# Performance work log

Hardware: AMD Instinct MI355X
Metric: run time of the kernel (lower is better)

## Reference

```python
import jax, jax.numpy as jnp
import numpy as np

CHUNK = 32
H = 4

def silu(x):
    return x * jax.nn.sigmoid(x)

def l2norm(x):
    return x * jax.lax.rsqrt(jnp.sum(x * x, -1, keepdims=True) + 1e-6)

def dwconv_causal(x_cl, w):
    # x_cl: (b, C, L), w: (C, k) depthwise causal conv (cross-correlation, left pad k-1)
    k = w.shape[1]
    xp = jnp.pad(x_cl, ((0, 0), (0, 0), (k - 1, 0)))
    return jax.lax.conv_general_dilated(xp, w[:, None, :], (1,), 'VALID',
        dimension_numbers=('NCH', 'OIH', 'NCH'), feature_group_count=x_cl.shape[1])

def short_conv_silu(x_bld, w):
    y = dwconv_causal(jnp.swapaxes(x_bld, 1, 2), w)
    return silu(jnp.swapaxes(y, 1, 2))

def delta_rule_chunkwise(q, k, v, beta, chunk=CHUNK):
    # q,k: (b,h,L,dk)  v: (b,h,L,dv)  beta: (b,h,L)
    b, h, L, dk = q.shape
    dv = v.shape[-1]
    pad = (-L) % chunk
    if pad:
        q, k, v = (jnp.pad(t, ((0, 0), (0, 0), (0, pad), (0, 0))) for t in (q, k, v))
        beta = jnp.pad(beta, ((0, 0), (0, 0), (0, pad)))
    n = (L + pad) // chunk
    q = l2norm(q)
    k = l2norm(k)
    v = v * beta[..., None]
    kb = k * beta[..., None]
    ch = lambda x: x.reshape(b, h, n, chunk, x.shape[-1])
    qc, kc, vc, kbc = map(ch, (q, k, v, kb))
    idx = jnp.arange(chunk)
    strict_lower = (idx[:, None] > idx[None, :]).astype(q.dtype)
    incl_lower = (idx[:, None] >= idx[None, :]).astype(q.dtype)
    # forward substitution to invert (I - tril(beta K K^T, -1)) per chunk
    attn = -jnp.einsum('bhncd,bhned->bhnce', kbc, kc) * strict_lower
    for i in range(1, chunk):
        upd = jnp.einsum('...j,...ji->...i', attn[..., i, :], attn[..., :, :i])
        attn = attn.at[..., i, :i].add(upd)
    attn = attn + jnp.eye(chunk, dtype=q.dtype)
    u = attn @ vc          # (b,h,n,c,dv)
    w = attn @ kbc         # (b,h,n,c,dk)
    xs = tuple(jnp.moveaxis(t, 2, 0) for t in (qc, kc, u, w))
    S0 = jnp.zeros((b, h, dk, dv), q.dtype)
    def step(S, x):
        qi, ki, ui, wi = x
        a_loc = jnp.einsum('bhcd,bhed->bhce', qi, ki) * incl_lower
        ui = ui - wi @ S
        oi = qi @ S + a_loc @ ui
        S = S + jnp.einsum('bhcd,bhcv->bhdv', ki, ui)
        return S, oi
    S, o = jax.lax.scan(step, S0, xs)
    o = jnp.moveaxis(o, 0, 2).reshape(b, h, n * chunk, dv)[:, :, :L]
    return o, S

def multiscale_conv(v, ms_w3, ms_w15, ms_w31, kernel_mix_w, channel_mixer_w):
    # v: (b,l,h,d)
    b, l, h, d = v.shape
    x = jnp.swapaxes(v.reshape(b, l, h * d), 1, 2)  # (b, h*d, l)
    outs = [dwconv_causal(x, w) for w in (ms_w3, ms_w15, ms_w31)]
    y = jnp.concatenate(outs, axis=1)               # (b, 3*h*d, l)
    # faithful to torch rearrange 'b (h kd) l -> b l h kd' on the concat layout
    y = y.reshape(b, h, 3 * d, l).transpose(0, 3, 1, 2)  # (b,l,h,3d)
    y = y @ kernel_mix_w                            # (b,l,h,d)
    y = (y.reshape(b, l, h * d) @ channel_mixer_w).reshape(b, l, h, d)
    return y

def _forward(hidden_states, Wq, Wk, Wv, Wb, conv_q_w, conv_k_w, conv_v_w,
             ms_w3, ms_w15, ms_w31, kernel_mix_w, channel_mixer_w,
             fusion_w1, fusion_b1, fusion_w2, fusion_b2, o_norm_w, Wo):
    b, L, D = hidden_states.shape
    h = H
    dk = Wq.shape[1] // h
    dv = Wv.shape[1] // h
    q = short_conv_silu(hidden_states @ Wq, conv_q_w).reshape(b, L, h, dk)
    k = short_conv_silu(hidden_states @ Wk, conv_k_w).reshape(b, L, h, dk)
    v = short_conv_silu(hidden_states @ Wv, conv_v_w).reshape(b, L, h, dv)
    v_direct = v
    beta = jax.nn.sigmoid(hidden_states @ Wb)  # (b,L,h)
    tr = lambda x: jnp.swapaxes(x, 1, 2)
    delta_out, _S = delta_rule_chunkwise(tr(q), tr(k), tr(v), tr(beta))
    delta_out = jnp.swapaxes(delta_out, 1, 2)  # (b,L,h,dv)
    ms_out = multiscale_conv(v_direct, ms_w3, ms_w15, ms_w31, kernel_mix_w, channel_mixer_w)
    bn = lambda x: jnp.mean(jnp.abs(x), -1)    # (b,L,h)
    gate_features = jnp.concatenate([hidden_states, bn(ms_out), bn(delta_out), bn(v_direct)], -1)
    hdn = jax.nn.gelu(gate_features @ fusion_w1 + fusion_b1, approximate=False)
    logits = (hdn @ fusion_w2 + fusion_b2).reshape(b, L, h, 3)
    wts = jax.nn.softmax(logits, -1)
    o = wts[..., 0:1] * ms_out + wts[..., 1:2] * delta_out + wts[..., 2:3] * v_direct
    o = o * jax.lax.rsqrt(jnp.mean(o * o, -1, keepdims=True) + 1e-5) * o_norm_w  # RMSNorm
    return o.reshape(b, L, h * dv) @ Wo

def setup_inputs() -> dict:
    B, L, D = 4, 2048, 1024
    h, d = H, D // H
    key = jax.random.key(0)
    ks = jax.random.split(key, 20)
    nrm = lambda k, shp, s: (jax.random.normal(k, shp, dtype=jnp.float32) * s)
    inp = {
        'hidden_states': nrm(ks[0], (B, L, D), 1.0),
        'Wq': nrm(ks[1], (D, D), D ** -0.5),
        'Wk': nrm(ks[2], (D, D), D ** -0.5),
        'Wv': nrm(ks[3], (D, D), D ** -0.5),
        'Wb': nrm(ks[4], (D, h), D ** -0.5),
        'conv_q_w': nrm(ks[5], (D, 4), 0.3),
        'conv_k_w': nrm(ks[6], (D, 4), 0.3),
        'conv_v_w': nrm(ks[7], (D, 4), 0.3),
        'ms_w3': nrm(ks[8], (D, 3), 0.02),
        'ms_w15': nrm(ks[9], (D, 15), 0.02),
        'ms_w31': nrm(ks[10], (D, 31), 0.02),
        'kernel_mix_w': nrm(ks[11], (3 * d, d), (3 * d) ** -0.5),
        'channel_mixer_w': nrm(ks[12], (D, D), D ** -0.5),
        'fusion_w1': nrm(ks[13], (D + 3 * h, 2 * D), (D + 3 * h) ** -0.5),
        'fusion_b1': jnp.zeros((2 * D,), jnp.float32),
        'fusion_w2': nrm(ks[14], (2 * D, 3 * h), (2 * D) ** -0.5),
        'fusion_b2': jnp.concatenate([jnp.zeros((2 * h,), jnp.float32), jnp.ones((h,), jnp.float32)]),
        'o_norm_w': jnp.ones((d,), jnp.float32),
        'Wo': nrm(ks[15], (D, D), D ** -0.5),
    }
    return inp

def reference(hidden_states, Wq, Wk, Wv, Wb, conv_q_w, conv_k_w, conv_v_w,
              ms_w3, ms_w15, ms_w31, kernel_mix_w, channel_mixer_w,
              fusion_w1, fusion_b1, fusion_w2, fusion_b2, o_norm_w, Wo):
    return _forward(hidden_states, Wq, Wk, Wv, Wb, conv_q_w, conv_k_w, conv_v_w,
                    ms_w3, ms_w15, ms_w31, kernel_mix_w, channel_mixer_w,
                    fusion_w1, fusion_b1, fusion_w2, fusion_b2, o_norm_w, Wo)
```

## Files before the change

kernel.cpp:

```cpp
#include <hip/hip_runtime.h>
#include <math.h>


typedef __attribute__((ext_vector_type(8))) __bf16 bf16x8;
typedef __attribute__((ext_vector_type(4))) float f32x4;

__device__ inline ushort f2bf(float f) {
    union { float f; unsigned u; } x; x.f = f;
    unsigned u = x.u;
    u += 0x7fffu + ((u >> 16) & 1u);
    return (ushort)(u >> 16);
}
__device__ inline float bf2f(ushort h) {
    union { unsigned u; float f; } x; x.u = ((unsigned)h) << 16;
    return x.f;
}
__device__ inline float ldf(float v) { return v; }
__device__ inline float ldf(ushort v) { return bf2f(v); }

template<int EPI>
__global__ __launch_bounds__(256) void gemm_mfma(
    const ushort* __restrict__ A, const ushort* __restrict__ BT,
    const float* __restrict__ bias, const float* __restrict__ extA,
    const float* __restrict__ extB, void* __restrict__ Cout,
    int M, int N, int K)
{
    __shared__ ushort As[2][128 * 32];
    __shared__ ushort Bs[2][128 * 32];
    __shared__ float bns[(EPI >= 2) ? 128 * 13 : 1];
    __shared__ float exb[(EPI >= 2) ? 12 * 128 : 1];
    const int tid = threadIdx.x;
    const int row0 = blockIdx.y * 128, col0 = blockIdx.x * 128;
    const int lane = tid & 63, wave = tid >> 6;
    const int wr = (wave >> 1) * 64, wc = (wave & 1) * 64;

    if (EPI >= 2) {
        for (int e = tid; e < 128 * 12; e += 256)
            bns[(e / 12) * 13 + (e % 12)] = extA[(long)(row0 + e / 12) * 12 + e % 12];
        for (int e = tid; e < 12 * 128; e += 256)
            exb[e] = extB[(long)(e >> 7) * N + col0 + (e & 127)];
    }

    f32x4 acc[4][4];
    #pragma unroll
    for (int m = 0; m < 4; ++m)
        #pragma unroll
        for (int n = 0; n < 4; ++n) {
            acc[m][n][0] = 0.f; acc[m][n][1] = 0.f;
            acc[m][n][2] = 0.f; acc[m][n][3] = 0.f;
        }

    const int rA = lane & 15;
    const int ko = (lane >> 4) * 8;
    const int srow = tid >> 2;
    const int skk = (tid & 3) * 8;

    for (int k0 = 0; k0 < K; k0 += 64) {
        #pragma unroll
        for (int hf = 0; hf < 2; ++hf) {
            #pragma unroll
            for (int i = 0; i < 2; ++i) {
                const long ga = (long)(row0 + i * 64 + srow) * K + k0 + hf * 32 + skk;
                __builtin_amdgcn_global_load_lds(
                    (const __attribute__((address_space(1))) void*)(A + ga),
                    (__attribute__((address_space(3))) void*)(&As[hf][0] + i * 2048 + wave * 512),
                    16, 0, 0);
                const long gb = (long)(col0 + i * 64 + srow) * K + k0 + hf * 32 + skk;
                __builtin_amdgcn_global_load_lds(
                    (const __attribute__((address_space(1))) void*)(BT + gb),
                    (__attribute__((address_space(3))) void*)(&Bs[hf][0] + i * 2048 + wave * 512),
                    16, 0, 0);
            }
        }
        __syncthreads();
        #pragma unroll
        for (int hf = 0; hf < 2; ++hf) {
            bf16x8 af[4], bfr[4];
            #pragma unroll
            for (int m = 0; m < 4; ++m)
                af[m] = *(const bf16x8*)(&As[hf][0] + (wr + m * 16 + rA) * 32 + ko);
            #pragma unroll
            for (int n = 0; n < 4; ++n)
                bfr[n] = *(const bf16x8*)(&Bs[hf][0] + (wc + n * 16 + rA) * 32 + ko);
            #pragma unroll
            for (int m = 0; m < 4; ++m)
                #pragma unroll
                for (int n = 0; n < 4; ++n)
                    acc[m][n] = __builtin_amdgcn_mfma_f32_16x16x32_bf16(af[m], bfr[n], acc[m][n], 0, 0, 0);
        }
        __syncthreads();
    }

    const int crow = (lane >> 4) * 4;
    const int ccol = lane & 15;
    #pragma unroll
    for (int m = 0; m < 4; ++m) {
        #pragma unroll
        for (int n = 0; n < 4; ++n) {
            #pragma unroll
            for (int r = 0; r < 4; ++r) {
                const int rl = wr + m * 16 + crow + r;
                const int cl = wc + n * 16 + ccol;
                float vv = acc[m][n][r];
                if (EPI >= 2) {
                    vv += bias[col0 + cl];
                    #pragma unroll
                    for (int j = 0; j < 12; ++j) vv += bns[rl * 13 + j] * exb[j * 128 + cl];
                    vv = 0.5f * vv * (1.f + erff(vv * 0.70710678118654752f));
                }
                const long off = (long)(row0 + rl) * N + col0 + cl;
                if (EPI == 0) ((float*)Cout)[off] = vv;
                else ((ushort*)Cout)[off] = f2bf(vv);
            }
        }
    }
}

__global__ __launch_bounds__(256) void transpose_cast(const float* __restrict__ W,
    ushort* __restrict__ WT, int K, int N)
{
    __shared__ float t[32][33];
    const int k0 = blockIdx.y * 32, n0 = blockIdx.x * 32;
    const int c = threadIdx.x & 31, r8 = threadIdx.x >> 5;
    #pragma unroll
    for (int rr = 0; rr < 4; ++rr) {
        const int r = r8 + rr * 8;
        t[r][c] = W[(long)(k0 + r) * N + n0 + c];
    }
    __syncthreads();
    #pragma unroll
    for (int rr = 0; rr < 4; ++rr) {
        const int r = r8 + rr * 8;
        WT[(long)(n0 + r) * K + k0 + c] = f2bf(t[c][r]);
    }
}

__global__ __launch_bounds__(256) void cast_bf16(const float* __restrict__ x,
    ushort* __restrict__ y)
{
    const long i = ((long)blockIdx.x * 256 + threadIdx.x) * 4;
    const float4 v = *(const float4*)(x + i);
    ushort4 o;
    o.x = f2bf(v.x); o.y = f2bf(v.y); o.z = f2bf(v.z); o.w = f2bf(v.w);
    *(ushort4*)(y + i) = o;
}

template<int NOUT, int MODE, typename TA>
__global__ __launch_bounds__(256) void gemm_smallN(const TA* __restrict__ A,
    const float* __restrict__ Bm, const float* __restrict__ bias,
    float* __restrict__ Cm, int K)
{
    __shared__ float part[4][NOUT];
    __shared__ float sm[NOUT];
    const int m = blockIdx.x, tid = threadIdx.x;
    const TA* ar = A + (long)m * K;
    float acc[NOUT];
    #pragma unroll
    for (int j = 0; j < NOUT; ++j) acc[j] = 0.f;
    for (int k = tid; k < K; k += 256) {
        const float a = ldf(ar[k]);
        #pragma unroll
        for (int j = 0; j < NOUT; ++j) acc[j] += a * Bm[(long)k * NOUT + j];
    }
    #pragma unroll
    for (int j = 0; j < NOUT; ++j)
        for (int off = 32; off > 0; off >>= 1) acc[j] += __shfl_down(acc[j], off);
    const int wid = tid >> 6, lane = tid & 63;
    if (lane == 0) {
        #pragma unroll
        for (int j = 0; j < NOUT; ++j) part[wid][j] = acc[j];
    }
    __syncthreads();
    if (tid < NOUT) {
        float s = part[0][tid] + part[1][tid] + part[2][tid] + part[3][tid];
        if (MODE == 0) {
            Cm[(long)m * NOUT + tid] = 1.f / (1.f + expf(-s));
        } else {
            sm[tid] = s + bias[tid];
        }
    }
    if (MODE == 1) {
        __syncthreads();
        if (tid < NOUT) {
            const int hh = tid / 3, r = tid - hh * 3;
            const float a0 = sm[hh * 3], a1 = sm[hh * 3 + 1], a2 = sm[hh * 3 + 2];
            const float mx = fmaxf(a0, fmaxf(a1, a2));
            const float e0 = expf(a0 - mx), e1 = expf(a1 - mx), e2 = expf(a2 - mx);
            const float mine = (r == 0) ? e0 : ((r == 1) ? e1 : e2);
            Cm[(long)m * NOUT + tid] = mine / (e0 + e1 + e2);
        }
    }
}

__global__ __launch_bounds__(256) void conv4_silu(const float* __restrict__ x,
    const float* __restrict__ wc, float* __restrict__ y)
{
    const long idx = (long)blockIdx.x * 256 + threadIdx.x;
    const int c = (int)(idx & 1023);
    const long bl = idx >> 10;
    const int l = (int)(bl & 2047);
    const long b = bl >> 11;
    const float* xp = x + b * 2048 * 1024 + c;
    const float* wp = wc + c * 4;
    float s = 0.f;
    #pragma unroll
    for (int t = 0; t < 4; ++t) {
        const int ll = l - 3 + t;
        if (ll >= 0) s += xp[(long)ll * 1024] * wp[t];
    }
    y[idx] = s / (1.f + expf(-s));
}

__global__ __launch_bounds__(256) void l2norm_bf16(const float* __restrict__ x,
    ushort* __restrict__ y)
{
    const long wid = ((long)blockIdx.x * 256 + threadIdx.x) >> 6;
    const int lane = threadIdx.x & 63;
    const float4 xv = *(const float4*)(x + wid * 256 + lane * 4);
    float ss = xv.x * xv.x + xv.y * xv.y + xv.z * xv.z + xv.w * xv.w;
    for (int off = 32; off > 0; off >>= 1) ss += __shfl_down(ss, off);
    ss = __shfl(ss, 0);
    const float inv = rsqrtf(ss + 1e-6f);
    ushort4 o;
    o.x = f2bf(xv.x * inv); o.y = f2bf(xv.y * inv);
    o.z = f2bf(xv.z * inv); o.w = f2bf(xv.w * inv);
    *(ushort4*)(y + wid * 256 + lane * 4) = o;
}

__global__ __launch_bounds__(256) void chunk_prep(
    const ushort* __restrict__ qn, const ushort* __restrict__ kn,
    const float* __restrict__ v, const float* __restrict__ beta,
    float* __restrict__ u, ushort* __restrict__ w16,
    ushort* __restrict__ kT16, ushort* __restrict__ al16)
{
    __shared__ float kb_s[32 * 256];
    __shared__ float bufB[32 * 256];
    __shared__ float Ms[32 * 33];
    __shared__ float Rs[32 * 33];
    __shared__ float bet[32];
    const int blk = blockIdx.x;
    const int n = blk & 63;
    const int bh = blk >> 6;
    const int h = bh & 3;
    const int b = bh >> 2;
    const int tid = threadIdx.x;
    const long lbase = (long)b * 2048 + n * 32;

    if (tid < 32) bet[tid] = beta[(lbase + tid) * 4 + h];
    __syncthreads();
    for (int e = tid; e < 8192; e += 256) {
        const int c = e >> 8, dd = e & 255;
        const float kv = bf2f(kn[(lbase + c) * 1024 + h * 256 + dd]);
        bufB[dd * 32 + c] = kv;
        kb_s[c * 256 + dd] = kv * bet[c];
    }
    __syncthreads();
    for (int e = tid; e < 8192; e += 256)
        kT16[(long)blk * 8192 + e] = f2bf(bufB[e]);

    const int j = tid & 31, i0 = tid >> 5;
    {
        float m4[4] = {0.f, 0.f, 0.f, 0.f};
        for (int dd = 0; dd < 256; ++dd) {
            const float kt = bufB[dd * 32 + j];
            #pragma unroll
            for (int ii = 0; ii < 4; ++ii) m4[ii] += kb_s[(i0 + 8 * ii) * 256 + dd] * kt;
        }
        #pragma unroll
        for (int ii = 0; ii < 4; ++ii) {
            const int i = i0 + 8 * ii;
            const float mv = (i > j) ? -m4[ii] : 0.f;
            Ms[i * 33 + j] = mv;
            Rs[i * 33 + j] = mv + ((i == j) ? 1.f : 0.f);
        }
    }
    {
        float a4[4] = {0.f, 0.f, 0.f, 0.f};
        for (int dd = 0; dd < 256; ++dd) {
            const float kt = bufB[dd * 32 + j];
            #pragma unroll
            for (int ii = 0; ii < 4; ++ii)
                a4[ii] += bf2f(qn[(lbase + (i0 + 8 * ii)) * 1024 + h * 256 + dd]) * kt;
        }
        #pragma unroll
        for (int ii = 0; ii < 4; ++ii) {
            const int i = i0 + 8 * ii;
            al16[(long)blk * 1024 + i * 32 + j] = f2bf((i >= j) ? a4[ii] : 0.f);
        }
    }
    __syncthreads();
    for (int it = 0; it < 4; ++it) {
        float p4[4] = {0.f, 0.f, 0.f, 0.f};
        for (int kk = 0; kk < 32; ++kk) {
            const float pb = Ms[kk * 33 + j];
            #pragma unroll
            for (int ii = 0; ii < 4; ++ii) p4[ii] += Ms[(i0 + 8 * ii) * 33 + kk] * pb;
        }
        __syncthreads();
        #pragma unroll
        for (int ii = 0; ii < 4; ++ii) Ms[(i0 + 8 * ii) * 33 + j] = p4[ii];
        __syncthreads();
        float r4[4] = {0.f, 0.f, 0.f, 0.f};
        for (int kk = 0; kk < 32; ++kk) {
            const float pb = Ms[kk * 33 + j];
            #pragma unroll
            for (int ii = 0; ii < 4; ++ii) r4[ii] += Rs[(i0 + 8 * ii) * 33 + kk] * pb;
        }
        __syncthreads();
        #pragma unroll
        for (int ii = 0; ii < 4; ++ii) Rs[(i0 + 8 * ii) * 33 + j] += r4[ii];
        __syncthreads();
    }
    for (int e = tid; e < 8192; e += 256) {
        const int c = e >> 8, dd = e & 255;
        bufB[c * 256 + dd] = v[(lbase + c) * 1024 + h * 256 + dd] * bet[c];
    }
    __syncthreads();
    {
        const int dd = tid;
        float accU[32], accW[32];
        #pragma unroll
        for (int r = 0; r < 32; ++r) { accU[r] = 0.f; accW[r] = 0.f; }
        for (int kk = 0; kk < 32; ++kk) {
            const float vv = bufB[kk * 256 + dd];
            const float bb = kb_s[kk * 256 + dd];
            #pragma unroll
            for (int r = 0; r < 32; ++r) {
                const float rr = Rs[r * 33 + kk];
                accU[r] += rr * vv;
                accW[r] += rr * bb;
            }
        }
        const long base = (long)blk * 32;
        #pragma unroll
        for (int r = 0; r < 32; ++r) {
            u  [(base + r) * 256 + dd] = accU[r];
            w16[(base + r) * 256 + dd] = f2bf(accW[r]);
        }
    }
}

__global__ __launch_bounds__(64, 1) void delta_scan_mfma(
    const ushort* __restrict__ q16, const ushort* __restrict__ kT16,
    const ushort* __restrict__ w16, const float* __restrict__ u,
    const ushort* __restrict__ al16, float* __restrict__ dt)
{
    __shared__ __align__(16) ushort Sb[16 * 264];
    __shared__ __align__(16) ushort Ub[16 * 40];
    const int blk = blockIdx.x;
    const int bh = blk & 15;
    const int sl = blk >> 4;
    const int h = bh & 3;
    const int b = bh >> 2;
    const int v0 = sl * 16;
    const int lane = threadIdx.x;
    const int col = lane & 15;
    const int grp = lane >> 4;

    const ushort* wp  = w16  + ((long)bh * 64 * 32 + col) * 256 + grp * 8;
    const ushort* qp  = q16  + ((long)b * 2048 + col) * 1024 + h * 256 + grp * 8;
    const ushort* kp  = kT16 + ((long)bh * 64 * 256 + col) * 32 + grp * 8;
    const ushort* ap  = al16 + ((long)bh * 64 * 32 + col) * 32 + grp * 8;
    const float*  Ug  = u    + ((long)bh * 64 * 32 + grp * 4) * 256 + v0 + col;
    float*        dp  = dt   + ((long)b * 2048 + grp * 4) * 1024 + h * 256 + v0 + col;

    f32x4 S[16];
    #pragma unroll
    for (int t = 0; t < 16; ++t) { S[t][0] = 0.f; S[t][1] = 0.f; S[t][2] = 0.f; S[t][3] = 0.f; }

    bf16x8 wf[2][8], qf[2][8], kf[16], alf[2], sf[8];
    float upre[8];

    #pragma unroll
    for (int kb = 0; kb < 8; ++kb)
        #pragma unroll
        for (int e = 0; e < 8; ++e) sf[kb][e] = (__bf16)0.f;

    #pragma unroll
    for (int rt = 0; rt < 2; ++rt)
        #pragma unroll
        for (int kb = 0; kb < 8; ++kb) {
            wf[rt][kb] = *(const bf16x8*)(wp + rt * 4096 + kb * 32);
            qf[rt][kb] = *(const bf16x8*)(qp + (long)rt * 16384 + kb * 32);
        }
    #pragma unroll
    for (int t = 0; t < 16; ++t) kf[t] = *(const bf16x8*)(kp + t * 512);
    alf[0] = *(const bf16x8*)(ap);
    alf[1] = *(const bf16x8*)(ap + 512);
    #pragma unroll
    for (int rt = 0; rt < 2; ++rt)
        #pragma unroll
        for (int r = 0; r < 4; ++r)
            upre[rt * 4 + r] = Ug[rt * 4096 + r * 256];

    for (int n = 0; n < 64; ++n) {
        f32x4 up[2];
        #pragma unroll
        for (int rt = 0; rt < 2; ++rt) {
            f32x4 a; a[0] = 0.f; a[1] = 0.f; a[2] = 0.f; a[3] = 0.f;
            #pragma unroll
            for (int kb = 0; kb < 8; ++kb)
                a = __builtin_amdgcn_mfma_f32_16x16x32_bf16(wf[rt][kb], sf[kb], a, 0, 0, 0);
            #pragma unroll
            for (int r = 0; r < 4; ++r)
                up[rt][r] = upre[rt * 4 + r] - a[r];
        }
        if (n < 63) {
            #pragma unroll
            for (int rt = 0; rt < 2; ++rt)
                #pragma unroll
                for (int kb = 0; kb < 8; ++kb)
                    wf[rt][kb] = *(const bf16x8*)(wp + (long)(n + 1) * 8192 + rt * 4096 + kb * 32);
        }

        #pragma unroll
        for (int rt = 0; rt < 2; ++rt) {
            ushort4 p;
            p.x = f2bf(up[rt][0]); p.y = f2bf(up[rt][1]);
            p.z = f2bf(up[rt][2]); p.w = f2bf(up[rt][3]);
            *(ushort4*)&Ub[col * 40 + rt * 16 + grp * 4] = p;
        }
        const bf16x8 uf = *(const bf16x8*)&Ub[col * 40 + grp * 8];

        #pragma unroll
        for (int rt = 0; rt < 2; ++rt) {
            f32x4 a; a[0] = 0.f; a[1] = 0.f; a[2] = 0.f; a[3] = 0.f;
            #pragma unroll
            for (int kb = 0; kb < 8; ++kb)
                a = __builtin_amdgcn_mfma_f32_16x16x32_bf16(qf[rt][kb], sf[kb], a, 0, 0, 0);
            a = __builtin_amdgcn_mfma_f32_16x16x32_bf16(alf[rt], uf, a, 0, 0, 0);
            #pragma unroll
            for (int r = 0; r < 4; ++r)
                dp[(long)n * 32768 + rt * 16384 + r * 1024] = a[r];
        }
        if (n < 63) {
            #pragma unroll
            for (int rt = 0; rt < 2; ++rt)
                #pragma unroll
                for (int kb = 0; kb < 8; ++kb)
                    qf[rt][kb] = *(const bf16x8*)(qp + (long)(n + 1) * 32768 + (long)rt * 16384 + kb * 32);
            alf[0] = *(const bf16x8*)(ap + (long)(n + 1) * 1024);
            alf[1] = *(const bf16x8*)(ap + (long)(n + 1) * 1024 + 512);
        }

        #pragma unroll
        for (int t = 0; t < 16; ++t)
            S[t] = __builtin_amdgcn_mfma_f32_16x16x32_bf16(kf[t], uf, S[t], 0, 0, 0);
        if (n < 63) {
            #pragma unroll
            for (int t = 0; t < 16; ++t)
                kf[t] = *(const bf16x8*)(kp + (long)(n + 1) * 8192 + t * 512);
            #pragma unroll
            for (int rt = 0; rt < 2; ++rt)
                #pragma unroll
                for (int r = 0; r < 4; ++r)
                    upre[rt * 4 + r] = Ug[(long)(n + 1) * 8192 + rt * 4096 + r * 256];
        }

        #pragma unroll
        for (int t = 0; t < 16; ++t) {
            ushort4 p;
            p.x = f2bf(S[t][0]); p.y = f2bf(S[t][1]);
            p.z = f2bf(S[t][2]); p.w = f2bf(S[t][3]);
            *(ushort4*)&Sb[col * 264 + t * 16 + grp * 4] = p;
        }
        #pragma unroll
        for (int kb = 0; kb < 8; ++kb)
            sf[kb] = *(const bf16x8*)&Sb[col * 264 + kb * 32 + grp * 8];
    }
}

__global__ __launch_bounds__(256) void ms_conv(const float* __restrict__ v,
    const float* __restrict__ w3, const float* __restrict__ w15,
    const float* __restrict__ w31, ushort* __restrict__ y)
{
    const int bid = blockIdx.x;
    const int b = bid >> 10;
    const int oct = (bid >> 2) & 255;
    const int c = ((bid & 3) << 8) + threadIdx.x;
    const int l0 = oct << 3;
    const float* vb = v + ((long)b * 2048) * 1024 + c;
    ushort* yb = y + ((long)b * 2048) * 3072 + c;

    float win[38];
    #pragma unroll
    for (int t = 0; t < 38; ++t) {
        const int ll = l0 - 30 + t;
        win[t] = (ll >= 0) ? vb[(long)ll * 1024] : 0.f;
    }
    {
        float W[31];
        #pragma unroll
        for (int t = 0; t < 31; ++t) W[t] = w31[c * 31 + t];
        #pragma unroll
        for (int j = 0; j < 8; ++j) {
            float s = 0.f;
            #pragma unroll
            for (int t = 0; t < 31; ++t) s += win[j + t] * W[t];
            yb[(long)(l0 + j) * 3072 + 2048] = f2bf(s);
        }
    }
    {
        float W[15];
        #pragma unroll
        for (int t = 0; t < 15; ++t) W[t] = w15[c * 15 + t];
        #pragma unroll
        for (int j = 0; j < 8; ++j) {
            float s = 0.f;
            #pragma unroll
            for (int t = 0; t < 15; ++t) s += win[j + 16 + t] * W[t];
            yb[(long)(l0 + j) * 3072 + 1024] = f2bf(s);
        }
    }
    {
        float W[3];
        #pragma unroll
        for (int t = 0; t < 3; ++t) W[t] = w3[c * 3 + t];
        #pragma unroll
        for (int j = 0; j < 8; ++j) {
            float s = 0.f;
            #pragma unroll
            for (int t = 0; t < 3; ++t) s += win[j + 28 + t] * W[t];
            yb[(long)(l0 + j) * 3072] = f2bf(s);
        }
    }
}

__global__ __launch_bounds__(256) void build_bn(const float* __restrict__ ms,
    const float* __restrict__ dt, const float* __restrict__ v,
    float* __restrict__ bn)
{
    const int bl = blockIdx.x, tid = threadIdx.x;
    const long rb = (long)bl * 1024;
    const int wid = tid >> 6, lane = tid & 63;
    const long base = rb + wid * 256 + lane * 4;
    float* g = bn + (long)bl * 12;
    float4 a;
    float s;
    a = *(const float4*)(ms + base);
    s = fabsf(a.x) + fabsf(a.y) + fabsf(a.z) + fabsf(a.w);
    for (int off = 32; off > 0; off >>= 1) s += __shfl_down(s, off);
    if (lane == 0) g[wid] = s * (1.f / 256.f);
    a = *(const float4*)(dt + base);
    s = fabsf(a.x) + fabsf(a.y) + fabsf(a.z) + fabsf(a.w);
    for (int off = 32; off > 0; off >>= 1) s += __shfl_down(s, off);
    if (lane == 0) g[4 + wid] = s * (1.f / 256.f);
    a = *(const float4*)(v + base);
    s = fabsf(a.x) + fabsf(a.y) + fabsf(a.z) + fabsf(a.w);
    for (int off = 32; off > 0; off >>= 1) s += __shfl_down(s, off);
    if (lane == 0) g[8 + wid] = s * (1.f / 256.f);
}

__global__ __launch_bounds__(256) void blend_rms(const float* __restrict__ ms,
    const float* __restrict__ dt, const float* __restrict__ v,
    const float* __restrict__ wts, const float* __restrict__ onw,
    ushort* __restrict__ o)
{
    const int bl = blockIdx.x, tid = threadIdx.x;
    const int wid = tid >> 6, lane = tid & 63;
    const long base = (long)bl * 1024 + wid * 256 + lane * 4;
    const float* wr = wts + (long)bl * 12 + wid * 3;
    const float w0 = wr[0], w1 = wr[1], w2 = wr[2];
    const float4 m = *(const float4*)(ms + base);
    const float4 d = *(const float4*)(dt + base);
    const float4 x = *(const float4*)(v + base);
    float4 ov;
    ov.x = w0 * m.x + w1 * d.x + w2 * x.x;
    ov.y = w0 * m.y + w1 * d.y + w2 * x.y;
    ov.z = w0 * m.z + w1 * d.z + w2 * x.z;
    ov.w = w0 * m.w + w1 * d.w + w2 * x.w;
    float ss = ov.x * ov.x + ov.y * ov.y + ov.z * ov.z + ov.w * ov.w;
    for (int off = 32; off > 0; off >>= 1) ss += __shfl_down(ss, off);
    ss = __shfl(ss, 0);
    const float inv = rsqrtf(ss * (1.f / 256.f) + 1e-5f);
    const float4 nw = *(const float4*)(onw + lane * 4);
    ushort4 ob;
    ob.x = f2bf(ov.x * inv * nw.x); ob.y = f2bf(ov.y * inv * nw.y);
    ob.z = f2bf(ov.z * inv * nw.z); ob.w = f2bf(ov.w * inv * nw.w);
    *(ushort4*)(o + base) = ob;
}

extern "C" void kernel_launch(void* const* d_in, const int* in_sizes, int n_in,
                              void* d_out, int out_size, void* d_ws, size_t ws_size,
                              hipStream_t stream)
{
    (void)in_sizes; (void)n_in; (void)out_size; (void)ws_size;
    const float* hid   = (const float*)d_in[0];
    const float* Wq    = (const float*)d_in[1];
    const float* Wk    = (const float*)d_in[2];
    const float* Wv    = (const float*)d_in[3];
    const float* Wb    = (const float*)d_in[4];
    const float* cq    = (const float*)d_in[5];
    const float* ck    = (const float*)d_in[6];
    const float* cv    = (const float*)d_in[7];
    const float* w3    = (const float*)d_in[8];
    const float* w15   = (const float*)d_in[9];
    const float* w31   = (const float*)d_in[10];
    const float* kmix  = (const float*)d_in[11];
    const float* cmix  = (const float*)d_in[12];
    const float* fw1   = (const float*)d_in[13];
    const float* fb1   = (const float*)d_in[14];
    const float* fw2   = (const float*)d_in[15];
    const float* fb2   = (const float*)d_in[16];
    const float* onw   = (const float*)d_in[17];
    const float* Wo    = (const float*)d_in[18];
    float* out = (float*)d_out;

    const size_t MiB = 1024 * 1024;
    char* W = (char*)d_ws;
    float*  s0    = (float*)(W);
    char*   s1c   = W + 32 * MiB;
    float*  s1    = (float*)s1c;
    float*  s2    = (float*)(W + 64 * MiB);
    char*   s3    = W + 96 * MiB;
    float*  s4    = (float*)(W + 128 * MiB);
    ushort* hid16 = (ushort*)(W + 160 * MiB);
    ushort* WqT   = (ushort*)(W + 176 * MiB);
    ushort* WkT   = WqT   + 1024 * 1024;
    ushort* WvT   = WkT   + 1024 * 1024;
    ushort* cmixT = WvT   + 1024 * 1024;
    ushort* WoT   = cmixT + 1024 * 1024;
    ushort* fw1T  = WoT   + 1024 * 1024;
    ushort* kmixT = fw1T  + 2048 * 1024;
    float*  beta  = (float*)(W + 191 * MiB);
    ushort* al16  = (ushort*)(W + 191 * MiB + 128 * 1024);
    float*  bnf   = (float*)(W + 193 * MiB + 128 * 1024);
    float*  wts   = bnf + 98304;

    ushort* q16    = (ushort*)s3;
    ushort* k16    = (ushort*)(s3 + 16 * MiB);
    ushort* mix16  = q16;
    ushort* ofin16 = k16;
    ushort* yms16  = (ushort*)s0;
    ushort* hdn16  = (ushort*)s0;
    float*  qlin = s0; float* qtmp = s1;
    float*  u = s0;
    ushort* w16  = (ushort*)s1c;
    ushort* kT16 = (ushort*)(s1c + 16 * MiB);
    float*  dt = s2; float* v = s4; float* msout = s1;

    const dim3 T256(256);
    cast_bf16<<<8192, T256, 0, stream>>>(hid, hid16);
    transpose_cast<<<dim3(32, 32), T256, 0, stream>>>(Wq, WqT, 1024, 1024);
    transpose_cast<<<dim3(32, 32), T256, 0, stream>>>(Wk, WkT, 1024, 1024);
    transpose_cast<<<dim3(32, 32), T256, 0, stream>>>(Wv, WvT, 1024, 1024);
    transpose_cast<<<dim3(32, 32), T256, 0, stream>>>(cmix, cmixT, 1024, 1024);
    transpose_cast<<<dim3(32, 32), T256, 0, stream>>>(Wo, WoT, 1024, 1024);
    transpose_cast<<<dim3(64, 32), T256, 0, stream>>>(fw1, fw1T, 1024, 2048);
    transpose_cast<<<dim3(8, 24), T256, 0, stream>>>(kmix, kmixT, 768, 256);
    gemm_mfma<0><<<dim3(8, 64), T256, 0, stream>>>(hid16, WqT, nullptr, nullptr, nullptr, qlin, 8192, 1024, 1024);
    conv4_silu<<<32768, T256, 0, stream>>>(qlin, cq, qtmp);
    l2norm_bf16<<<8192, T256, 0, stream>>>(qtmp, q16);
    gemm_mfma<0><<<dim3(8, 64), T256, 0, stream>>>(hid16, WkT, nullptr, nullptr, nullptr, qlin, 8192, 1024, 1024);
    conv4_silu<<<32768, T256, 0, stream>>>(qlin, ck, qtmp);
    l2norm_bf16<<<8192, T256, 0, stream>>>(qtmp, k16);
    gemm_mfma<0><<<dim3(8, 64), T256, 0, stream>>>(hid16, WvT, nullptr, nullptr, nullptr, qlin, 8192, 1024, 1024);
    conv4_silu<<<32768, T256, 0, stream>>>(qlin, cv, v);
    gemm_smallN<4, 0><<<8192, T256, 0, stream>>>(hid, Wb, nullptr, beta, 1024);
    chunk_prep<<<1024, T256, 0, stream>>>(q16, k16, v, beta, u, w16, kT16, al16);
    delta_scan_mfma<<<256, dim3(64), 0, stream>>>(q16, kT16, w16, u, al16, dt);
    ms_conv<<<4096, T256, 0, stream>>>(v, w3, w15, w31, yms16);
    gemm_mfma<1><<<dim3(2, 256), T256, 0, stream>>>(yms16, kmixT, nullptr, nullptr, nullptr, mix16, 32768, 256, 768);
    gemm_mfma<0><<<dim3(8, 64), T256, 0, stream>>>(mix16, cmixT, nullptr, nullptr, nullptr, msout, 8192, 1024, 1024);
    build_bn<<<8192, T256, 0, stream>>>(msout, dt, v, bnf);
    gemm_mfma<3><<<dim3(16, 64), T256, 0, stream>>>(hid16, fw1T, fb1, bnf, fw1 + 1024L * 2048, hdn16, 8192, 2048, 1024);
    gemm_smallN<12, 1><<<8192, T256, 0, stream>>>(hdn16, fw2, fb2, wts, 2048);
    blend_rms<<<8192, T256, 0, stream>>>(msout, dt, v, wts, onw, ofin16);
    gemm_mfma<0><<<dim3(8, 64), T256, 0, stream>>>(ofin16, WoT, nullptr, nullptr, nullptr, out, 8192, 1024, 1024);
}
```

Measured before the change: 773.3 us.

## Use MFMA for chunk KK^T and QK^T, stage k/v in LDS with vector loads

In chunk_prep, the two scalar 32x32x256 dot-product loops (beta*K K^T and Q K^T) are replaced with bf16 MFMA 16x16x32 instructions, one 16x16 tile per wave. K and beta-scaled K are kept in LDS as padded bf16, and v*beta is preloaded with float4 loads up front, which removes a later sync phase. The aim is to cut scalar FMA and LDS work in the prep kernel. In exchange, beta*K is rounded to bf16 before it is used in both the inverse and the W product, which loses some precision, and the kT16 transpose now reads LDS with a strided pattern.

```diff
diff --git a/kernel.cpp b/kernel.cpp
--- a/kernel.cpp
+++ b/kernel.cpp
@@ -233,8 +233,9 @@
     float* __restrict__ u, ushort* __restrict__ w16,
     ushort* __restrict__ kT16, ushort* __restrict__ al16)
 {
-    __shared__ float kb_s[32 * 256];
-    __shared__ float bufB[32 * 256];
+    __shared__ __align__(16) ushort kn16[32 * 264];
+    __shared__ __align__(16) ushort kb16[32 * 264];
+    __shared__ __align__(16) float  vb[32 * 260];
     __shared__ float Ms[32 * 33];
     __shared__ float Rs[32 * 33];
     __shared__ float bet[32];
@@ -248,47 +249,68 @@
 
     if (tid < 32) bet[tid] = beta[(lbase + tid) * 4 + h];
     __syncthreads();
-    for (int e = tid; e < 8192; e += 256) {
-        const int c = e >> 8, dd = e & 255;
-        const float kv = bf2f(kn[(lbase + c) * 1024 + h * 256 + dd]);
-        bufB[dd * 32 + c] = kv;
-        kb_s[c * 256 + dd] = kv * bet[c];
+
+    #pragma unroll
+    for (int it = 0; it < 4; ++it) {
+        const int e2 = tid + it * 256;
+        const int c = e2 >> 5, d8 = (e2 & 31) * 8;
+        const uint4 kv = *(const uint4*)(kn + (lbase + c) * 1024 + h * 256 + d8);
+        *(uint4*)&kn16[c * 264 + d8] = kv;
+        const float bc = bet[c];
+        uint4 kb;
+        kb.x = (uint)f2bf(bf2f((ushort)(kv.x & 0xffffu)) * bc) |
+               ((uint)f2bf(bf2f((ushort)(kv.x >> 16)) * bc) << 16);
+        kb.y = (uint)f2bf(bf2f((ushort)(kv.y & 0xffffu)) * bc) |
+               ((uint)f2bf(bf2f((ushort)(kv.y >> 16)) * bc) << 16);
+        kb.z = (uint)f2bf(bf2f((ushort)(kv.z & 0xffffu)) * bc) |
+               ((uint)f2bf(bf2f((ushort)(kv.z >> 16)) * bc) << 16);
+        kb.w = (uint)f2bf(bf2f((ushort)(kv.w & 0xffffu)) * bc) |
+               ((uint)f2bf(bf2f((ushort)(kv.w >> 16)) * bc) << 16);
+        *(uint4*)&kb16[c * 264 + d8] = kb;
+    }
+    #pragma unroll
+    for (int it = 0; it < 8; ++it) {
+        const int e2 = tid + it * 256;
+        const int c = e2 >> 6, d4 = (e2 & 63) * 4;
+        float4 vv = *(const float4*)(v + (lbase + c) * 1024 + h * 256 + d4);
+        const float bc = bet[c];
+        vv.x *= bc; vv.y *= bc; vv.z *= bc; vv.w *= bc;
+        *(float4*)&vb[c * 260 + d4] = vv;
     }
     __syncthreads();
+
     for (int e = tid; e < 8192; e += 256)
-        kT16[(long)blk * 8192 + e] = f2bf(bufB[e]);
-
-    const int j = tid & 31, i0 = tid >> 5;
+        kT16[(long)blk * 8192 + e] = kn16[(e & 31) * 264 + (e >> 5)];
+
+    const int lane = tid & 63, wave = tid >> 6;
+    const int wr2 = (wave >> 1) * 16, wc2 = (wave & 1) * 16;
+    const int rA = lane & 15, ko = (lane >> 4) * 8;
     {
-        float m4[4] = {0.f, 0.f, 0.f, 0.f};
-        for (int dd = 0; dd < 256; ++dd) {
-            const float kt = bufB[dd * 32 + j];
-            #pragma unroll
-            for (int ii = 0; ii < 4; ++ii) m4[ii] += kb_s[(i0 + 8 * ii) * 256 + dd] * kt;
-        }
-        #pragma unroll
-        for (int ii = 0; ii < 4; ++ii) {
-            const int i = i0 + 8 * ii;
-            const float mv = (i > j) ? -m4[ii] : 0.f;
+        f32x4 accM, accA;
+        accM[0] = 0.f; accM[1] = 0.f; accM[2] = 0.f; accM[3] = 0.f;
+        accA[0] = 0.f; accA[1] = 0.f; accA[2] = 0.f; accA[3] = 0.f;
+        const ushort* qrow = qn + (lbase + wr2 + rA) * 1024 + h * 256 + ko;
+        #pragma unroll
+        for (int ks = 0; ks < 8; ++ks) {
+            const bf16x8 bfK = *(const bf16x8*)&kn16[(wc2 + rA) * 264 + ks * 32 + ko];
+            const bf16x8 afM = *(const bf16x8*)&kb16[(wr2 + rA) * 264 + ks * 32 + ko];
+            accM = __builtin_amdgcn_mfma_f32_16x16x32_bf16(afM, bfK, accM, 0, 0, 0);
+            const bf16x8 afQ = *(const bf16x8*)(qrow + ks * 32);
+            accA = __builtin_amdgcn_mfma_f32_16x16x32_bf16(afQ, bfK, accA, 0, 0, 0);
+        }
+        const int ccol = lane & 15, crow = (lane >> 4) * 4;
+        #pragma unroll
+        for (int r = 0; r < 4; ++r) {
+            const int i = wr2 + crow + r, j = wc2 + ccol;
+            const float mv = (i > j) ? -accM[r] : 0.f;
             Ms[i * 33 + j] = mv;
             Rs[i * 33 + j] = mv + ((i == j) ? 1.f : 0.f);
-        }
-    }
-    {
-        float a4[4] = {0.f, 0.f, 0.f, 0.f};
-        for (int dd = 0; dd < 256; ++dd) {
-            const float kt = bufB[dd * 32 + j];
-            #pragma unroll
-            for (int ii = 0; ii < 4; ++ii)
-                a4[ii] += bf2f(qn[(lbase + (i0 + 8 * ii)) * 1024 + h * 256 + dd]) * kt;
-        }
-        #pragma unroll
-        for (int ii = 0; ii < 4; ++ii) {
-            const int i = i0 + 8 * ii;
-            al16[(long)blk * 1024 + i * 32 + j] = f2bf((i >= j) ? a4[ii] : 0.f);
+            al16[(long)blk * 1024 + i * 32 + j] = f2bf((i >= j) ? accA[r] : 0.f);
         }
     }
     __syncthreads();
+
+    const int j = tid & 31, i0 = tid >> 5;
     for (int it = 0; it < 4; ++it) {
         float p4[4] = {0.f, 0.f, 0.f, 0.f};
         for (int kk = 0; kk < 32; ++kk) {
@@ -311,19 +333,15 @@
         for (int ii = 0; ii < 4; ++ii) Rs[(i0 + 8 * ii) * 33 + j] += r4[ii];
         __syncthreads();
     }
-    for (int e = tid; e < 8192; e += 256) {
-        const int c = e >> 8, dd = e & 255;
-        bufB[c * 256 + dd] = v[(lbase + c) * 1024 + h * 256 + dd] * bet[c];
-    }
-    __syncthreads();
+
     {
         const int dd = tid;
         float accU[32], accW[32];
         #pragma unroll
         for (int r = 0; r < 32; ++r) { accU[r] = 0.f; accW[r] = 0.f; }
         for (int kk = 0; kk < 32; ++kk) {
-            const float vv = bufB[kk * 256 + dd];
-            const float bb = kb_s[kk * 256 + dd];
+            const float vv = vb[kk * 260 + dd];
+            const float bb = bf2f(kb16[kk * 264 + dd]);
             #pragma unroll
             for (int r = 0; r < 32; ++r) {
                 const float rr = Rs[r * 33 + kk];
```

New measurement: 722.0 us. 6.6% less time.
